# Kernel optimization log

Hardware: AMD Instinct MI355X
Metric: run time of the kernel (lower is better)

The kernel has to match this reference:

```python
import jax, jax.numpy as jnp
import numpy as np

D_ATOM, D_MODEL, H = 128, 512, 4
D_H = D_ATOM // H
D_FF = 4 * D_ATOM
EPS = 1e-5


def _ln(x, g, b):
    m = jnp.mean(x, axis=-1, keepdims=True)
    v = jnp.mean((x - m) ** 2, axis=-1, keepdims=True)
    return (x - m) / jnp.sqrt(v + EPS) * g + b


def setup_inputs() -> dict:
    key = jax.random.key(0)
    ks = jax.random.split(key, 20)
    B, N_ATOM, N_PAIRS, N_TOK = 2, 2048, 16384, 512
    c_atom = jax.random.normal(ks[0], (B, N_ATOM, D_ATOM), dtype=jnp.float32)
    p_lm = jax.random.normal(ks[1], (B, N_PAIRS, 16), dtype=jnp.float32)
    p_lm_idx = jax.random.randint(ks[2], (B, N_PAIRS, 2), 0, N_ATOM, dtype=jnp.int32)
    token_idx = jnp.sort(jax.random.randint(ks[3], (B, N_ATOM), 0, N_TOK, dtype=jnp.int32), axis=-1)
    s = 0.05
    w = lambda k, sh: jax.random.normal(k, sh, dtype=jnp.float32) * s
    return {
        'c_atom': c_atom, 'p_lm': p_lm, 'p_lm_idx': p_lm_idx,
        'token_idx': token_idx, 'n_tokens': N_TOK,
        'ln_attn_g': jnp.ones((D_ATOM,), jnp.float32), 'ln_attn_b': jnp.zeros((D_ATOM,), jnp.float32),
        'w_q': w(ks[4], (D_ATOM, D_ATOM)), 'w_k': w(ks[5], (D_ATOM, D_ATOM)),
        'w_v': w(ks[6], (D_ATOM, D_ATOM)), 'w_g': w(ks[7], (D_ATOM, D_ATOM)),
        'w_o': w(ks[8], (D_ATOM, D_ATOM)),
        'pb_w': w(ks[9], (16, H)), 'pb_b': jnp.zeros((H,), jnp.float32),
        'ln_ff_g': jnp.ones((D_ATOM,), jnp.float32), 'ln_ff_b': jnp.zeros((D_ATOM,), jnp.float32),
        'sw_w1': w(ks[10], (D_ATOM, D_FF)), 'sw_w2': w(ks[11], (D_ATOM, D_FF)),
        'sw_w3': w(ks[12], (D_FF, D_ATOM)),
        'tok_w': w(ks[13], (D_ATOM, D_MODEL)), 'tok_b': jnp.zeros((D_MODEL,), jnp.float32),
    }


def reference(c_atom, p_lm, p_lm_idx, token_idx, n_tokens,
              ln_attn_g, ln_attn_b, w_q, w_k, w_v, w_g, w_o, pb_w, pb_b,
              ln_ff_g, ln_ff_b, sw_w1, sw_w2, sw_w3, tok_w, tok_b):
    B, N, _ = c_atom.shape
    q_n = _ln(c_atom, ln_attn_g, ln_attn_b)
    Q = (q_n @ w_q).reshape(B, N, H, D_H)
    K = (q_n @ w_k).reshape(B, N, H, D_H)
    V = (q_n @ w_v).reshape(B, N, H, D_H)
    G = q_n @ w_g  # (B, N, d_atom)

    scores = jnp.einsum('bihd,bjhd->bhij', Q, K) / jnp.sqrt(jnp.float32(D_H))

    bias = p_lm @ pb_w + pb_b  # (B, P, H)
    def scat(src, dst, b_):
        return jnp.zeros((H, N, N), b_.dtype).at[:, src, dst].set(b_.T)
    pair_bias = jax.vmap(scat)(p_lm_idx[..., 0], p_lm_idx[..., 1], bias)
    scores = scores + pair_bias

    token_mask = token_idx[:, :, None] == token_idx[:, None, :]  # (B,N,N)
    scores = jnp.where(token_mask[:, None], scores, -jnp.inf)
    attn = jax.nn.softmax(scores, axis=-1)
    attn = jnp.nan_to_num(attn)

    att_out = jnp.einsum('bhij,bjhd->bihd', attn, V).reshape(B, N, D_ATOM)
    q = c_atom + jax.nn.sigmoid(G) * (att_out @ w_o)
    h = _ln(q, ln_ff_g, ln_ff_b)
    q = q + (jax.nn.silu(h @ sw_w1) * (h @ sw_w2)) @ sw_w3
    atom_feat = q @ tok_w + tok_b  # (B, N, d_model)

    seg = (token_idx + jnp.arange(B, dtype=token_idx.dtype)[:, None] * n_tokens).reshape(-1)
    sums = jax.ops.segment_sum(atom_feat.reshape(B * N, D_MODEL), seg, num_segments=B * n_tokens)
    cnts = jax.ops.segment_sum(jnp.ones((B * N,), atom_feat.dtype), seg, num_segments=B * n_tokens)
    out = sums / jnp.maximum(cnts, 1.0)[:, None]
    return out.reshape(B, n_tokens, D_MODEL)
```

## Files before the change

kernel.cpp:

```cpp
#include <hip/hip_runtime.h>
#include <hip/hip_bf16.h>
#include <math.h>

#define B_     2
#define N_     2048
#define DA     128
#define H_     4
#define DH     32
#define DFF    512
#define DM     512
#define NT     512
#define NP     16384
#define MAXL   32
#define LDSP   136

typedef short bf16x8 __attribute__((ext_vector_type(8)));
typedef float f32x4  __attribute__((ext_vector_type(4)));

__device__ __forceinline__ short bf16r(float x) {
    union { float f; unsigned u; } v; v.f = x;
    unsigned r = v.u + 0x7FFFu + ((v.u >> 16) & 1u);
    return (short)(r >> 16);
}

__global__ __launch_bounds__(1024) void setup_kernel(
        const float* __restrict__ wq, const float* __restrict__ wk,
        const float* __restrict__ wv, const float* __restrict__ wg,
        const float* __restrict__ wo, const float* __restrict__ w1,
        const float* __restrict__ w2, const float* __restrict__ w3,
        const float* __restrict__ tw, const int* __restrict__ tok,
        short* __restrict__ pqkvg, short* __restrict__ pwo,
        short* __restrict__ pw12, short* __restrict__ pw3,
        short* __restrict__ ptok,
        int* __restrict__ cnt, int* __restrict__ tst) {
    __shared__ int c[1024];
    __shared__ int sb[1024];
    if (blockIdx.x < 42) {
        int gid = blockIdx.x * 1024 + threadIdx.x;
        int lane = gid & 63;
        int grp = gid >> 6;
        int quad = lane >> 4, nn = lane & 15;
        const float* src; short* dst; int stride;
        if (grp < 128) {
            int g = grp; int kt = g & 3, nt = g >> 2;
            int n = nt * 16 + nn;
            const float* w = (n < 128) ? wq : (n < 256) ? wk : (n < 384) ? wv : wg;
            src = w + (kt * 32 + quad * 8) * 128 + (n & 127);
            dst = pqkvg + (g * 64 + lane) * 8;
            stride = 128;
        } else if (grp < 160) {
            int g = grp - 128; int kt = g & 3, nt = g >> 2;
            src = wo + (kt * 32 + quad * 8) * 128 + nt * 16 + nn;
            dst = pwo + (g * 64 + lane) * 8;
            stride = 128;
        } else if (grp < 416) {
            int g = grp - 160; int kt = g & 3, nt = g >> 2;
            int n = nt * 16 + nn;
            src = ((n & 1) ? w2 : w1) + (kt * 32 + quad * 8) * 512 + (n >> 1);
            dst = pw12 + (g * 64 + lane) * 8;
            stride = 512;
        } else if (grp < 544) {
            int g = grp - 416; int kt = g & 15, nt = g >> 4;
            src = w3 + (kt * 32 + quad * 8) * 128 + nt * 16 + nn;
            dst = pw3 + (g * 64 + lane) * 8;
            stride = 128;
        } else {
            int g = grp - 544; int kt = g & 3, nt = g >> 2;
            src = tw + (kt * 32 + quad * 8) * 512 + nt * 16 + nn;
            dst = ptok + (g * 64 + lane) * 8;
            stride = 512;
        }
#pragma unroll
        for (int j = 0; j < 8; j++) dst[j] = bf16r(src[j * stride]);
    } else {
        int tid = threadIdx.x;
        c[tid] = 0;
        __syncthreads();
#pragma unroll
        for (int i = 0; i < 4; i++) {
            int idx = tid + i * 1024;
            int b = idx >> 11;
            atomicAdd(&c[b * NT + tok[idx]], 1);
        }
        __syncthreads();
        int t = tid & (NT - 1);
        int v = c[tid];
        int* cur = c;
        int* alt = sb;
        for (int d = 1; d < NT; d <<= 1) {
            int y = cur[tid];
            if (t >= d) y += cur[tid - d];
            alt[tid] = y;
            __syncthreads();
            int* tmp = cur; cur = alt; alt = tmp;
        }
        tst[tid] = cur[tid] - v;
        cnt[tid] = v;
    }
}

__device__ __forceinline__ void ln_to_lds(const float* __restrict__ x,
                                          const float* __restrict__ g,
                                          const float* __restrict__ b,
                                          short* __restrict__ lds) {
    int t = threadIdx.x;
    int row = t >> 2, sub = t & 3;
    const float* xr = x + row * DA + sub * 32;
    float4 v[8];
    float s = 0.f, sq = 0.f;
#pragma unroll
    for (int i = 0; i < 8; i++) {
        v[i] = *(const float4*)(xr + i * 4);
        s  += v[i].x + v[i].y + v[i].z + v[i].w;
        sq += v[i].x * v[i].x + v[i].y * v[i].y + v[i].z * v[i].z + v[i].w * v[i].w;
    }
    s += __shfl_xor(s, 1); sq += __shfl_xor(sq, 1);
    s += __shfl_xor(s, 2); sq += __shfl_xor(sq, 2);
    float mean = s * (1.f / 128.f);
    float var = sq * (1.f / 128.f) - mean * mean;
    float inv = rsqrtf(var + 1e-5f);
    const float* gp = g + sub * 32;
    const float* bp = b + sub * 32;
    short* dst = lds + row * LDSP + sub * 32;
#pragma unroll
    for (int i = 0; i < 8; i++) {
        dst[i * 4 + 0] = bf16r((v[i].x - mean) * inv * gp[i * 4 + 0] + bp[i * 4 + 0]);
        dst[i * 4 + 1] = bf16r((v[i].y - mean) * inv * gp[i * 4 + 1] + bp[i * 4 + 1]);
        dst[i * 4 + 2] = bf16r((v[i].z - mean) * inv * gp[i * 4 + 2] + bp[i * 4 + 2]);
        dst[i * 4 + 3] = bf16r((v[i].w - mean) * inv * gp[i * 4 + 3] + bp[i * 4 + 3]);
    }
}

template<int K, int NTT>
__device__ __forceinline__ void gemm_lds(const short* __restrict__ Alds,
                                         const short* __restrict__ Bp,
                                         int nt0, int lane, f32x4* acc) {
    constexpr int KT = K / 32;
    const short* arow = Alds + (lane & 15) * LDSP + (lane >> 4) * 8;
    const short* bbase = Bp + nt0 * KT * 512 + lane * 8;
#pragma unroll
    for (int kt = 0; kt < KT; kt++) {
        bf16x8 a = *(const bf16x8*)(arow + kt * 32);
#pragma unroll
        for (int nt = 0; nt < NTT; nt++) {
            bf16x8 b = *(const bf16x8*)(bbase + (nt * KT + kt) * 512);
            acc[nt] = __builtin_amdgcn_mfma_f32_16x16x32_bf16(a, b, acc[nt], 0, 0, 0);
        }
    }
}

template<int K>
__device__ __forceinline__ void gemm_glb(const short* __restrict__ A,
                                         const short* __restrict__ Bp,
                                         int m0, int nt0, int lane, f32x4 acc[4]) {
    constexpr int KT = K / 32;
    const short* arow = A + (m0 + (lane & 15)) * K + (lane >> 4) * 8;
    const short* bbase = Bp + nt0 * KT * 512 + lane * 8;
#pragma unroll
    for (int kt = 0; kt < KT; kt++) {
        bf16x8 a = *(const bf16x8*)(arow + kt * 32);
#pragma unroll
        for (int nt = 0; nt < 4; nt++) {
            bf16x8 b = *(const bf16x8*)(bbase + (nt * KT + kt) * 512);
            acc[nt] = __builtin_amdgcn_mfma_f32_16x16x32_bf16(a, b, acc[nt], 0, 0, 0);
        }
    }
}

__global__ __launch_bounds__(256) void lnqkvg_mfma(const float* __restrict__ c_atom,
                                                   const float* __restrict__ lg,
                                                   const float* __restrict__ lb,
                                                   const short* __restrict__ Bp,
                                                   float* __restrict__ out) {
    __shared__ short alds[64 * LDSP];
    int base = blockIdx.x * 64;
    ln_to_lds(c_atom + base * DA, lg, lb, alds);
    __syncthreads();
    int lane = threadIdx.x & 63;
    int wave = threadIdx.x >> 6;
    int nt0 = blockIdx.y * 8;
    f32x4 acc[8];
#pragma unroll
    for (int i = 0; i < 8; i++)
#pragma unroll
        for (int r = 0; r < 4; r++) acc[i][r] = 0.f;
    gemm_lds<128, 8>(alds + wave * 16 * LDSP, Bp, nt0, lane, acc);
    int r0 = base + wave * 16 + ((lane >> 4) << 2);
    int cc = lane & 15;
#pragma unroll
    for (int nt = 0; nt < 8; nt++) {
        int col = (nt0 + nt) * 16 + cc;
#pragma unroll
        for (int r = 0; r < 4; r++) out[(r0 + r) * 512 + col] = acc[nt][r];
    }
}

__global__ __launch_bounds__(256) void lnffn1_mfma(const float* __restrict__ qbuf,
                                                   const float* __restrict__ lg,
                                                   const float* __restrict__ lb,
                                                   const short* __restrict__ Bp,
                                                   short* __restrict__ u) {
    __shared__ short alds[64 * LDSP];
    int base = blockIdx.x * 64;
    ln_to_lds(qbuf + base * DA, lg, lb, alds);
    __syncthreads();
    int lane = threadIdx.x & 63;
    int wave = threadIdx.x >> 6;
    int nt0 = blockIdx.y * 16;
    f32x4 acc[16];
#pragma unroll
    for (int i = 0; i < 16; i++)
#pragma unroll
        for (int r = 0; r < 4; r++) acc[i][r] = 0.f;
    gemm_lds<128, 16>(alds + wave * 16 * LDSP, Bp, nt0, lane, acc);
    int r0 = base + wave * 16 + ((lane >> 4) << 2);
    int cc = lane & 15;
#pragma unroll
    for (int nt = 0; nt < 16; nt++) {
        int col8 = (nt0 + nt) * 8 + (cc >> 1);
#pragma unroll
        for (int r = 0; r < 4; r++) {
            float v = acc[nt][r];
            float p = __shfl_xor(v, 1);
            if (!(lane & 1)) {
                float sil = v / (1.f + expf(-v));
                u[(r0 + r) * DFF + col8] = bf16r(sil * p);
            }
        }
    }
}

__global__ __launch_bounds__(128) void outproj_mfma(const short* __restrict__ atth,
                                                    const short* __restrict__ Bp,
                                                    const float* __restrict__ qkvg,
                                                    const float* __restrict__ c_atom,
                                                    float* __restrict__ qbuf) {
    int lane = threadIdx.x & 63;
    int m0 = blockIdx.x * 32 + (threadIdx.x >> 6) * 16;
    int nt0 = blockIdx.y * 4;
    f32x4 acc[4];
#pragma unroll
    for (int i = 0; i < 4; i++)
#pragma unroll
        for (int r = 0; r < 4; r++) acc[i][r] = 0.f;
    gemm_glb<128>(atth, Bp, m0, nt0, lane, acc);
    int r0 = m0 + ((lane >> 4) << 2);
    int cc = lane & 15;
#pragma unroll
    for (int nt = 0; nt < 4; nt++) {
        int col = (nt0 + nt) * 16 + cc;
#pragma unroll
        for (int r = 0; r < 4; r++) {
            int row = r0 + r;
            float g = qkvg[row * 512 + 384 + col];
            float sg = 1.f / (1.f + expf(-g));
            qbuf[row * DA + col] = c_atom[row * DA + col] + sg * acc[nt][r];
        }
    }
}

__global__ __launch_bounds__(128) void ffn2_mfma(const short* __restrict__ u,
                                                 const short* __restrict__ Bp,
                                                 const float* __restrict__ qbuf,
                                                 short* __restrict__ q2h) {
    int lane = threadIdx.x & 63;
    int m0 = blockIdx.x * 32 + (threadIdx.x >> 6) * 16;
    int nt0 = blockIdx.y * 4;
    f32x4 acc[4];
#pragma unroll
    for (int i = 0; i < 4; i++)
#pragma unroll
        for (int r = 0; r < 4; r++) acc[i][r] = 0.f;
    gemm_glb<512>(u, Bp, m0, nt0, lane, acc);
    int r0 = m0 + ((lane >> 4) << 2);
    int cc = lane & 15;
#pragma unroll
    for (int nt = 0; nt < 4; nt++) {
        int col = (nt0 + nt) * 16 + cc;
#pragma unroll
        for (int r = 0; r < 4; r++) {
            int row = r0 + r;
            q2h[row * DA + col] = bf16r(qbuf[row * DA + col] + acc[nt][r]);
        }
    }
}

__global__ __launch_bounds__(256) void tokproj_mfma(const short* __restrict__ q2h,
                                                    const short* __restrict__ Bp,
                                                    const float* __restrict__ tb,
                                                    float* __restrict__ af) {
    int lane = threadIdx.x & 63;
    int m0 = blockIdx.x * 64 + (threadIdx.x >> 6) * 16;
    int nt0 = blockIdx.y * 4;
    f32x4 acc[4];
#pragma unroll
    for (int i = 0; i < 4; i++)
#pragma unroll
        for (int r = 0; r < 4; r++) acc[i][r] = 0.f;
    gemm_glb<128>(q2h, Bp, m0, nt0, lane, acc);
    int r0 = m0 + ((lane >> 4) << 2);
    int cc = lane & 15;
#pragma unroll
    for (int nt = 0; nt < 4; nt++) {
        int col = (nt0 + nt) * 16 + cc;
        float bv = tb[col];
#pragma unroll
        for (int r = 0; r < 4; r++) af[(r0 + r) * DM + col] = acc[nt][r] + bv;
    }
}

__global__ void pair_win_kernel(const int* __restrict__ pidx,
                                const int* __restrict__ tok,
                                const int* __restrict__ tst,
                                int* __restrict__ winner) {
    int p = blockIdx.x * 256 + threadIdx.x;
    if (p >= B_ * NP) return;
    int b = p >> 14, pp = p & (NP - 1);
    int src = pidx[p * 2], dst = pidx[p * 2 + 1];
    int ts = tok[b * N_ + src], td = tok[b * N_ + dst];
    if (ts == td) {
        int jj = dst - tst[b * NT + td];
        if (jj < MAXL) atomicMax(&winner[(b * N_ + src) * MAXL + jj], pp + 1);
    }
}

__global__ __launch_bounds__(128) void attn_kernel(const float* __restrict__ qkvg,
                                                   const int* __restrict__ tok,
                                                   const int* __restrict__ tst,
                                                   const int* __restrict__ cnt,
                                                   const int* __restrict__ winner,
                                                   const float* __restrict__ plm,
                                                   const float* __restrict__ pbw,
                                                   const float* __restrict__ pbb,
                                                   short* __restrict__ atth) {
    __shared__ float sc[H_][MAXL];
    int blk = blockIdx.x;
    int b = blk >> 11;
    int h = threadIdx.x >> 5, d = threadIdx.x & 31;
    int t = tok[blk];
    int start = tst[b * NT + t];
    int L = cnt[b * NT + t];
    if (L > MAXL) L = MAXL;
    float qv = qkvg[blk * 512 + h * DH + d];
    const float scale = 0.17677669529663687f;
    for (int jj = 0; jj < L; jj++) {
        int j = b * N_ + start + jj;
        float kv = qkvg[j * 512 + 128 + h * DH + d];
        float s = qv * kv;
#pragma unroll
        for (int m = 16; m; m >>= 1) s += __shfl_xor(s, m, 32);
        s *= scale;
        int pp1 = winner[blk * MAXL + jj];
        if (pp1 > 0) {
            const float* pl = plm + (b * NP + pp1 - 1) * 16;
            float bsum = pbb[h];
#pragma unroll
            for (int f = 0; f < 16; f++) bsum += pl[f] * pbw[f * H_ + h];
            s += bsum;
        }
        if (d == 0) sc[h][jj] = s;
    }
    __syncthreads();
    float mx = -1e30f;
    for (int jj = 0; jj < L; jj++) mx = fmaxf(mx, sc[h][jj]);
    float denom = 0.f, acc = 0.f;
    for (int jj = 0; jj < L; jj++) {
        float pj = expf(sc[h][jj] - mx);
        denom += pj;
        acc += pj * qkvg[(b * N_ + start + jj) * 512 + 256 + h * DH + d];
    }
    atth[blk * DA + h * DH + d] = bf16r(acc / denom);
}

__global__ __launch_bounds__(128) void segmean_kernel(const float* __restrict__ af,
                                                      const int* __restrict__ tst,
                                                      const int* __restrict__ cnt,
                                                      float* __restrict__ out) {
    int blk = blockIdx.x;
    int b = blk >> 9;
    int tid = threadIdx.x;
    int start = tst[blk], n = cnt[blk];
    float acc[4] = {0.f, 0.f, 0.f, 0.f};
    for (int a = 0; a < n; a++) {
        const float* row = af + (b * N_ + start + a) * DM;
#pragma unroll
        for (int c = 0; c < 4; c++) acc[c] += row[tid + c * 128];
    }
    float inv = 1.f / fmaxf((float)n, 1.f);
#pragma unroll
    for (int c = 0; c < 4; c++) out[(size_t)blk * DM + tid + c * 128] = acc[c] * inv;
}

extern "C" void kernel_launch(void* const* d_in, const int* in_sizes, int n_in,
                              void* d_out, int out_size, void* d_ws, size_t ws_size,
                              hipStream_t stream) {
    const float* c_atom  = (const float*)d_in[0];
    const float* p_lm    = (const float*)d_in[1];
    const int*   p_idx   = (const int*)d_in[2];
    const int*   tok     = (const int*)d_in[3];
    const float* ln_a_g  = (const float*)d_in[5];
    const float* ln_a_b  = (const float*)d_in[6];
    const float* w_q     = (const float*)d_in[7];
    const float* w_k     = (const float*)d_in[8];
    const float* w_v     = (const float*)d_in[9];
    const float* w_g     = (const float*)d_in[10];
    const float* w_o     = (const float*)d_in[11];
    const float* pb_w    = (const float*)d_in[12];
    const float* pb_b    = (const float*)d_in[13];
    const float* ln_f_g  = (const float*)d_in[14];
    const float* ln_f_b  = (const float*)d_in[15];
    const float* sw_w1   = (const float*)d_in[16];
    const float* sw_w2   = (const float*)d_in[17];
    const float* sw_w3   = (const float*)d_in[18];
    const float* tok_w   = (const float*)d_in[19];
    const float* tok_b   = (const float*)d_in[20];
    float* out = (float*)d_out;

    float* ws = (float*)d_ws;
    int*   cnt   = (int*)ws;
    int*   tst   = cnt + 1024;
    int*   win   = tst + 1024;
    short* pqkvg = (short*)(win + 131072);
    short* pwo   = pqkvg + 65536;
    short* pw12  = pwo + 16384;
    short* pw3   = pw12 + 131072;
    short* ptok  = pw3 + 65536;
    short* atth  = ptok + 65536;
    float* qbuf  = (float*)(atth + 524288);
    float* qkvg  = qbuf + 524288;
    float* af    = qkvg + 2097152;
    short* uh    = (short*)qkvg;
    short* q2h   = atth;

    setup_kernel<<<43, 1024, 0, stream>>>(w_q, w_k, w_v, w_g, w_o, sw_w1, sw_w2,
                                          sw_w3, tok_w, tok,
                                          pqkvg, pwo, pw12, pw3, ptok, cnt, tst);

    lnqkvg_mfma<<<dim3(64, 4), 256, 0, stream>>>(c_atom, ln_a_g, ln_a_b, pqkvg, qkvg);
    pair_win_kernel<<<B_ * NP / 256, 256, 0, stream>>>(p_idx, tok, tst, win);

    attn_kernel<<<B_ * N_, 128, 0, stream>>>(qkvg, tok, tst, cnt, win,
                                             p_lm, pb_w, pb_b, atth);
    outproj_mfma<<<dim3(128, 2), 128, 0, stream>>>(atth, pwo, qkvg, c_atom, qbuf);

    lnffn1_mfma<<<dim3(64, 4), 256, 0, stream>>>(qbuf, ln_f_g, ln_f_b, pw12, uh);
    ffn2_mfma<<<dim3(128, 2), 128, 0, stream>>>(uh, pw3, qbuf, q2h);
    tokproj_mfma<<<dim3(64, 8), 256, 0, stream>>>(q2h, ptok, tok_b, af);

    segmean_kernel<<<B_ * NT, 128, 0, stream>>>(af, tst, cnt, out);
}
```

Measured before the change: 164.2 us.

## Fuse out-proj with FFN1, fold pair-window into setup, project token means

The pair-winner scatter moves into extra blocks of the setup kernel and is indexed by dst&31, so it no longer needs the token start offsets. The output projection, gating, residual, second LayerNorm and SwiGLU first layer are merged into one kernel that keeps its rows in registers and LDS. The token segment mean is now taken over the bf16 residual stream before the token projection, which shrinks that GEMM to 1024 rows and removes the large per-atom feature buffer. The goal is fewer launches and less global traffic, at the cost of redundant out-projection work across blockIdx.y, bf16 rounding of the means, and giving empty tokens the bias rather than zero.

```diff
diff --git a/kernel.cpp b/kernel.cpp
--- a/kernel.cpp
+++ b/kernel.cpp
@@ -22,6 +22,11 @@
     unsigned r = v.u + 0x7FFFu + ((v.u >> 16) & 1u);
     return (short)(r >> 16);
 }
+__device__ __forceinline__ float bf2f(short h) {
+    union { unsigned u; float f; } v;
+    v.u = ((unsigned)(unsigned short)h) << 16;
+    return v.f;
+}
 
 __global__ __launch_bounds__(1024) void setup_kernel(
         const float* __restrict__ wq, const float* __restrict__ wk,
@@ -29,10 +34,12 @@
         const float* __restrict__ wo, const float* __restrict__ w1,
         const float* __restrict__ w2, const float* __restrict__ w3,
         const float* __restrict__ tw, const int* __restrict__ tok,
+        const int* __restrict__ pidx,
         short* __restrict__ pqkvg, short* __restrict__ pwo,
         short* __restrict__ pw12, short* __restrict__ pw3,
         short* __restrict__ ptok,
-        int* __restrict__ cnt, int* __restrict__ tst) {
+        int* __restrict__ cnt, int* __restrict__ tst,
+        int* __restrict__ win) {
     __shared__ int c[1024];
     __shared__ int sb[1024];
     if (blockIdx.x < 42) {
@@ -72,7 +79,7 @@
         }
 #pragma unroll
         for (int j = 0; j < 8; j++) dst[j] = bf16r(src[j * stride]);
-    } else {
+    } else if (blockIdx.x == 42) {
         int tid = threadIdx.x;
         c[tid] = 0;
         __syncthreads();
@@ -96,6 +103,12 @@
         }
         tst[tid] = cur[tid] - v;
         cnt[tid] = v;
+    } else {
+        int p = (blockIdx.x - 43) * 1024 + threadIdx.x;
+        int b = p >> 14, pp = p & (NP - 1);
+        int src = pidx[p * 2], dst = pidx[p * 2 + 1];
+        if (tok[b * N_ + src] == tok[b * N_ + dst])
+            atomicMax(&win[(b * N_ + src) * MAXL + (dst & 31)], pp + 1);
     }
 }
 
@@ -149,10 +162,10 @@
     }
 }
 
-template<int K>
+template<int K, int NTT>
 __device__ __forceinline__ void gemm_glb(const short* __restrict__ A,
                                          const short* __restrict__ Bp,
-                                         int m0, int nt0, int lane, f32x4 acc[4]) {
+                                         int m0, int nt0, int lane, f32x4* acc) {
     constexpr int KT = K / 32;
     const short* arow = A + (m0 + (lane & 15)) * K + (lane >> 4) * 8;
     const short* bbase = Bp + nt0 * KT * 512 + lane * 8;
@@ -160,7 +173,7 @@
     for (int kt = 0; kt < KT; kt++) {
         bf16x8 a = *(const bf16x8*)(arow + kt * 32);
 #pragma unroll
-        for (int nt = 0; nt < 4; nt++) {
+        for (int nt = 0; nt < NTT; nt++) {
             bf16x8 b = *(const bf16x8*)(bbase + (nt * KT + kt) * 512);
             acc[nt] = __builtin_amdgcn_mfma_f32_16x16x32_bf16(a, b, acc[nt], 0, 0, 0);
         }
@@ -192,135 +205,6 @@
         int col = (nt0 + nt) * 16 + cc;
 #pragma unroll
         for (int r = 0; r < 4; r++) out[(r0 + r) * 512 + col] = acc[nt][r];
-    }
-}
-
-__global__ __launch_bounds__(256) void lnffn1_mfma(const float* __restrict__ qbuf,
-                                                   const float* __restrict__ lg,
-                                                   const float* __restrict__ lb,
-                                                   const short* __restrict__ Bp,
-                                                   short* __restrict__ u) {
-    __shared__ short alds[64 * LDSP];
-    int base = blockIdx.x * 64;
-    ln_to_lds(qbuf + base * DA, lg, lb, alds);
-    __syncthreads();
-    int lane = threadIdx.x & 63;
-    int wave = threadIdx.x >> 6;
-    int nt0 = blockIdx.y * 16;
-    f32x4 acc[16];
-#pragma unroll
-    for (int i = 0; i < 16; i++)
-#pragma unroll
-        for (int r = 0; r < 4; r++) acc[i][r] = 0.f;
-    gemm_lds<128, 16>(alds + wave * 16 * LDSP, Bp, nt0, lane, acc);
-    int r0 = base + wave * 16 + ((lane >> 4) << 2);
-    int cc = lane & 15;
-#pragma unroll
-    for (int nt = 0; nt < 16; nt++) {
-        int col8 = (nt0 + nt) * 8 + (cc >> 1);
-#pragma unroll
-        for (int r = 0; r < 4; r++) {
-            float v = acc[nt][r];
-            float p = __shfl_xor(v, 1);
-            if (!(lane & 1)) {
-                float sil = v / (1.f + expf(-v));
-                u[(r0 + r) * DFF + col8] = bf16r(sil * p);
-            }
-        }
-    }
-}
-
-__global__ __launch_bounds__(128) void outproj_mfma(const short* __restrict__ atth,
-                                                    const short* __restrict__ Bp,
-                                                    const float* __restrict__ qkvg,
-                                                    const float* __restrict__ c_atom,
-                                                    float* __restrict__ qbuf) {
-    int lane = threadIdx.x & 63;
-    int m0 = blockIdx.x * 32 + (threadIdx.x >> 6) * 16;
-    int nt0 = blockIdx.y * 4;
-    f32x4 acc[4];
-#pragma unroll
-    for (int i = 0; i < 4; i++)
-#pragma unroll
-        for (int r = 0; r < 4; r++) acc[i][r] = 0.f;
-    gemm_glb<128>(atth, Bp, m0, nt0, lane, acc);
-    int r0 = m0 + ((lane >> 4) << 2);
-    int cc = lane & 15;
-#pragma unroll
-    for (int nt = 0; nt < 4; nt++) {
-        int col = (nt0 + nt) * 16 + cc;
-#pragma unroll
-        for (int r = 0; r < 4; r++) {
-            int row = r0 + r;
-            float g = qkvg[row * 512 + 384 + col];
-            float sg = 1.f / (1.f + expf(-g));
-            qbuf[row * DA + col] = c_atom[row * DA + col] + sg * acc[nt][r];
-        }
-    }
-}
-
-__global__ __launch_bounds__(128) void ffn2_mfma(const short* __restrict__ u,
-                                                 const short* __restrict__ Bp,
-                                                 const float* __restrict__ qbuf,
-                                                 short* __restrict__ q2h) {
-    int lane = threadIdx.x & 63;
-    int m0 = blockIdx.x * 32 + (threadIdx.x >> 6) * 16;
-    int nt0 = blockIdx.y * 4;
-    f32x4 acc[4];
-#pragma unroll
-    for (int i = 0; i < 4; i++)
-#pragma unroll
-        for (int r = 0; r < 4; r++) acc[i][r] = 0.f;
-    gemm_glb<512>(u, Bp, m0, nt0, lane, acc);
-    int r0 = m0 + ((lane >> 4) << 2);
-    int cc = lane & 15;
-#pragma unroll
-    for (int nt = 0; nt < 4; nt++) {
-        int col = (nt0 + nt) * 16 + cc;
-#pragma unroll
-        for (int r = 0; r < 4; r++) {
-            int row = r0 + r;
-            q2h[row * DA + col] = bf16r(qbuf[row * DA + col] + acc[nt][r]);
-        }
-    }
-}
-
-__global__ __launch_bounds__(256) void tokproj_mfma(const short* __restrict__ q2h,
-                                                    const short* __restrict__ Bp,
-                                                    const float* __restrict__ tb,
-                                                    float* __restrict__ af) {
-    int lane = threadIdx.x & 63;
-    int m0 = blockIdx.x * 64 + (threadIdx.x >> 6) * 16;
-    int nt0 = blockIdx.y * 4;
-    f32x4 acc[4];
-#pragma unroll
-    for (int i = 0; i < 4; i++)
-#pragma unroll
-        for (int r = 0; r < 4; r++) acc[i][r] = 0.f;
-    gemm_glb<128>(q2h, Bp, m0, nt0, lane, acc);
-    int r0 = m0 + ((lane >> 4) << 2);
-    int cc = lane & 15;
-#pragma unroll
-    for (int nt = 0; nt < 4; nt++) {
-        int col = (nt0 + nt) * 16 + cc;
-        float bv = tb[col];
-#pragma unroll
-        for (int r = 0; r < 4; r++) af[(r0 + r) * DM + col] = acc[nt][r] + bv;
-    }
-}
-
-__global__ void pair_win_kernel(const int* __restrict__ pidx,
-                                const int* __restrict__ tok,
-                                const int* __restrict__ tst,
-                                int* __restrict__ winner) {
-    int p = blockIdx.x * 256 + threadIdx.x;
-    if (p >= B_ * NP) return;
-    int b = p >> 14, pp = p & (NP - 1);
-    int src = pidx[p * 2], dst = pidx[p * 2 + 1];
-    int ts = tok[b * N_ + src], td = tok[b * N_ + dst];
-    if (ts == td) {
-        int jj = dst - tst[b * NT + td];
-        if (jj < MAXL) atomicMax(&winner[(b * N_ + src) * MAXL + jj], pp + 1);
     }
 }
 
@@ -350,7 +234,7 @@
 #pragma unroll
         for (int m = 16; m; m >>= 1) s += __shfl_xor(s, m, 32);
         s *= scale;
-        int pp1 = winner[blk * MAXL + jj];
+        int pp1 = winner[blk * MAXL + ((start + jj) & 31)];
         if (pp1 > 0) {
             const float* pl = plm + (b * NP + pp1 - 1) * 16;
             float bsum = pbb[h];
@@ -372,23 +256,165 @@
     atth[blk * DA + h * DH + d] = bf16r(acc / denom);
 }
 
-__global__ __launch_bounds__(128) void segmean_kernel(const float* __restrict__ af,
-                                                      const int* __restrict__ tst,
-                                                      const int* __restrict__ cnt,
-                                                      float* __restrict__ out) {
-    int blk = blockIdx.x;
-    int b = blk >> 9;
+__global__ __launch_bounds__(256) void oplnffn1_mfma(const short* __restrict__ atth,
+                                                     const short* __restrict__ pwo,
+                                                     const float* __restrict__ qkvg,
+                                                     const float* __restrict__ c_atom,
+                                                     const float* __restrict__ lg,
+                                                     const float* __restrict__ lb,
+                                                     const short* __restrict__ pw12,
+                                                     float* __restrict__ qbuf,
+                                                     short* __restrict__ u) {
+    __shared__ short alds[64 * LDSP];
+    int lane = threadIdx.x & 63;
+    int wave = threadIdx.x >> 6;
+    int base = blockIdx.x * 64;
+    int m0 = base + wave * 16;
+    int quad = lane >> 4, cc = lane & 15;
+
+    f32x4 acc[8];
+#pragma unroll
+    for (int i = 0; i < 8; i++)
+#pragma unroll
+        for (int r = 0; r < 4; r++) acc[i][r] = 0.f;
+    gemm_glb<128, 8>(atth, pwo, m0, 0, lane, acc);
+
+    float rsum[4], rsq[4];
+#pragma unroll
+    for (int r = 0; r < 4; r++) {
+        int row = m0 + quad * 4 + r;
+        float s = 0.f, sq = 0.f;
+#pragma unroll
+        for (int nt = 0; nt < 8; nt++) {
+            int col = nt * 16 + cc;
+            float g = qkvg[row * 512 + 384 + col];
+            float sg = 1.f / (1.f + expf(-g));
+            float val = c_atom[row * DA + col] + sg * acc[nt][r];
+            acc[nt][r] = val;
+            s += val; sq += val * val;
+            if (blockIdx.y == 0) qbuf[row * DA + col] = val;
+        }
+        rsum[r] = s; rsq[r] = sq;
+    }
+#pragma unroll
+    for (int m = 1; m < 16; m <<= 1) {
+#pragma unroll
+        for (int r = 0; r < 4; r++) {
+            rsum[r] += __shfl_xor(rsum[r], m);
+            rsq[r]  += __shfl_xor(rsq[r], m);
+        }
+    }
+#pragma unroll
+    for (int r = 0; r < 4; r++) {
+        float mean = rsum[r] * (1.f / 128.f);
+        float var = rsq[r] * (1.f / 128.f) - mean * mean;
+        float inv = rsqrtf(var + 1e-5f);
+        int lrow = wave * 16 + quad * 4 + r;
+#pragma unroll
+        for (int nt = 0; nt < 8; nt++) {
+            int col = nt * 16 + cc;
+            alds[lrow * LDSP + col] = bf16r((acc[nt][r] - mean) * inv * lg[col] + lb[col]);
+        }
+    }
+    __syncthreads();
+
+    int nt0 = blockIdx.y * 16;
+    f32x4 acc2[16];
+#pragma unroll
+    for (int i = 0; i < 16; i++)
+#pragma unroll
+        for (int r = 0; r < 4; r++) acc2[i][r] = 0.f;
+    gemm_lds<128, 16>(alds + wave * 16 * LDSP, pw12, nt0, lane, acc2);
+    int r0 = m0 + quad * 4;
+#pragma unroll
+    for (int nt = 0; nt < 16; nt++) {
+        int col8 = (nt0 + nt) * 8 + (cc >> 1);
+#pragma unroll
+        for (int r = 0; r < 4; r++) {
+            float v = acc2[nt][r];
+            float p = __shfl_xor(v, 1);
+            if (!(lane & 1)) {
+                float sil = v / (1.f + expf(-v));
+                u[(r0 + r) * DFF + col8] = bf16r(sil * p);
+            }
+        }
+    }
+}
+
+__global__ __launch_bounds__(128) void ffn2_mfma(const short* __restrict__ u,
+                                                 const short* __restrict__ Bp,
+                                                 const float* __restrict__ qbuf,
+                                                 short* __restrict__ q2h) {
+    int lane = threadIdx.x & 63;
+    int m0 = blockIdx.x * 32 + (threadIdx.x >> 6) * 16;
+    int nt0 = blockIdx.y * 4;
+    f32x4 acc[4];
+#pragma unroll
+    for (int i = 0; i < 4; i++)
+#pragma unroll
+        for (int r = 0; r < 4; r++) acc[i][r] = 0.f;
+    gemm_glb<512, 4>(u, Bp, m0, nt0, lane, acc);
+    int r0 = m0 + ((lane >> 4) << 2);
+    int cc = lane & 15;
+#pragma unroll
+    for (int nt = 0; nt < 4; nt++) {
+        int col = (nt0 + nt) * 16 + cc;
+#pragma unroll
+        for (int r = 0; r < 4; r++) {
+            int row = r0 + r;
+            q2h[row * DA + col] = bf16r(qbuf[row * DA + col] + acc[nt][r]);
+        }
+    }
+}
+
+__global__ __launch_bounds__(256) void tokmean_mfma(const short* __restrict__ q2h,
+                                                    const int* __restrict__ tst,
+                                                    const int* __restrict__ cnt,
+                                                    const short* __restrict__ Bp,
+                                                    const float* __restrict__ tb,
+                                                    float* __restrict__ out) {
+    __shared__ short alds[64 * LDSP];
     int tid = threadIdx.x;
-    int start = tst[blk], n = cnt[blk];
-    float acc[4] = {0.f, 0.f, 0.f, 0.f};
+    int tt = tid >> 2, sub = tid & 3;
+    int token = blockIdx.x * 64 + tt;
+    int start = tst[token], n = cnt[token];
+    int b = token >> 9;
+    float accm[32];
+#pragma unroll
+    for (int i = 0; i < 32; i++) accm[i] = 0.f;
     for (int a = 0; a < n; a++) {
-        const float* row = af + (b * N_ + start + a) * DM;
-#pragma unroll
-        for (int c = 0; c < 4; c++) acc[c] += row[tid + c * 128];
-    }
-    float inv = 1.f / fmaxf((float)n, 1.f);
-#pragma unroll
-    for (int c = 0; c < 4; c++) out[(size_t)blk * DM + tid + c * 128] = acc[c] * inv;
+        const short* rp = q2h + (b * N_ + start + a) * DA + sub * 32;
+#pragma unroll
+        for (int v8 = 0; v8 < 4; v8++) {
+            bf16x8 v = *(const bf16x8*)(rp + v8 * 8);
+#pragma unroll
+            for (int j = 0; j < 8; j++) accm[v8 * 8 + j] += bf2f(v[j]);
+        }
+    }
+    float inv = (n > 0) ? 1.f / (float)n : 0.f;
+    short* dst = alds + tt * LDSP + sub * 32;
+#pragma unroll
+    for (int i = 0; i < 32; i++) dst[i] = bf16r(accm[i] * inv);
+    __syncthreads();
+
+    int lane = tid & 63;
+    int wave = tid >> 6;
+    int nt0 = blockIdx.y * 4;
+    f32x4 acc[4];
+#pragma unroll
+    for (int i = 0; i < 4; i++)
+#pragma unroll
+        for (int r = 0; r < 4; r++) acc[i][r] = 0.f;
+    gemm_lds<128, 4>(alds + wave * 16 * LDSP, Bp, nt0, lane, acc);
+    int r0 = blockIdx.x * 64 + wave * 16 + ((lane >> 4) << 2);
+    int cc = lane & 15;
+#pragma unroll
+    for (int nt = 0; nt < 4; nt++) {
+        int col = (nt0 + nt) * 16 + cc;
+        float bv = tb[col];
+#pragma unroll
+        for (int r = 0; r < 4; r++) out[(size_t)(r0 + r) * DM + col] = acc[nt][r] + bv;
+    }
 }
 
 extern "C" void kernel_launch(void* const* d_in, const int* in_sizes, int n_in,
@@ -428,24 +454,23 @@
     short* atth  = ptok + 65536;
     float* qbuf  = (float*)(atth + 524288);
     float* qkvg  = qbuf + 524288;
-    float* af    = qkvg + 2097152;
-    short* uh    = (short*)qkvg;
+    short* uh    = (short*)(qkvg + 2097152);
     short* q2h   = atth;
 
-    setup_kernel<<<43, 1024, 0, stream>>>(w_q, w_k, w_v, w_g, w_o, sw_w1, sw_w2,
-                                          sw_w3, tok_w, tok,
-                                          pqkvg, pwo, pw12, pw3, ptok, cnt, tst);
+    setup_kernel<<<75, 1024, 0, stream>>>(w_q, w_k, w_v, w_g, w_o, sw_w1, sw_w2,
+                                          sw_w3, tok_w, tok, p_idx,
+                                          pqkvg, pwo, pw12, pw3, ptok,
+                                          cnt, tst, win);
 
     lnqkvg_mfma<<<dim3(64, 4), 256, 0, stream>>>(c_atom, ln_a_g, ln_a_b, pqkvg, qkvg);
-    pair_win_kernel<<<B_ * NP / 256, 256, 0, stream>>>(p_idx, tok, tst, win);
 
     attn_kernel<<<B_ * N_, 128, 0, stream>>>(qkvg, tok, tst, cnt, win,
                                              p_lm, pb_w, pb_b, atth);
-    outproj_mfma<<<dim3(128, 2), 128, 0, stream>>>(atth, pwo, qkvg, c_atom, qbuf);
-
-    lnffn1_mfma<<<dim3(64, 4), 256, 0, stream>>>(qbuf, ln_f_g, ln_f_b, pw12, uh);
+
+    oplnffn1_mfma<<<dim3(64, 4), 256, 0, stream>>>(atth, pwo, qkvg, c_atom,
+                                                   ln_f_g, ln_f_b, pw12, qbuf, uh);
+
     ffn2_mfma<<<dim3(128, 2), 128, 0, stream>>>(uh, pw3, qbuf, q2h);
-    tokproj_mfma<<<dim3(64, 8), 256, 0, stream>>>(q2h, ptok, tok_b, af);
-
-    segmean_kernel<<<B_ * NT, 128, 0, stream>>>(af, tst, cnt, out);
-}
+
+    tokmean_mfma<<<dim3(16, 8), 256, 0, stream>>>(q2h, tst, cnt, ptok, tok_b, out);
+}
```

After: 162.0 us (median of 2 runs). About the same (-1.3%).
